# Performance work log

Hardware: AMD Instinct MI355X
Metric: run time of the kernel (lower is better)

Reference implementation:

```python
import jax, jax.numpy as jnp
import numpy as np

N0, N1, N2, K, D, H = 131072, 16384, 4096, 8, 256, 256
LN_EPS = 1e-5
BN_EPS = 1e-5


def _lstm_last(x, W_ih, W_hh, b_ih, b_hh):
    # x: [N, K, Din]; returns final hidden state [N, Hh] (DGL lstm aggregator)
    N = x.shape[0]
    Hh = W_hh.shape[1]

    def step(carry, xt):
        h, c = carry
        z = xt @ W_ih.T + b_ih + h @ W_hh.T + b_hh  # [N, 4*Hh]
        i, f, g, o = jnp.split(z, 4, axis=-1)
        c = jax.nn.sigmoid(f) * c + jax.nn.sigmoid(i) * jnp.tanh(g)
        h = jax.nn.sigmoid(o) * jnp.tanh(c)
        return (h, c), None

    init = (jnp.zeros((N, Hh), x.dtype), jnp.zeros((N, Hh), x.dtype))
    (h, _), _ = jax.lax.scan(step, init, jnp.swapaxes(x, 0, 1))
    return h


def _sage_lstm(h_src, idx, W_ih, W_hh, b_ih, b_hh, W_self, W_neigh, b_neigh):
    # DGL SAGEConv(aggregator='lstm'), eval mode (feat_drop = identity).
    n_dst = idx.shape[0]
    h_self = h_src[:n_dst]                  # DGL block: dst nodes are first rows of src
    nbrs = jnp.take(h_src, idx, axis=0)     # [n_dst, K, Din] neighbor gather
    h_n = _lstm_last(nbrs, W_ih, W_hh, b_ih, b_hh)
    # fc_self has no bias, fc_neigh has bias (DGL); activation = exact GELU
    return jax.nn.gelu(h_self @ W_self.T + h_n @ W_neigh.T + b_neigh, approximate=False)


def _layernorm(x, g, b):
    mu = jnp.mean(x, -1, keepdims=True)
    var = jnp.mean((x - mu) ** 2, -1, keepdims=True)
    return (x - mu) * jax.lax.rsqrt(var + LN_EPS) * g + b


def _forward(h0, idx0, idx1,
             W_ih1, W_hh1, b_ih1, b_hh1, W_self1, W_neigh1, b_neigh1,
             W_ih2, W_hh2, b_ih2, b_hh2, W_self2, W_neigh2, b_neigh2,
             ln_g, ln_b, bn_g, bn_b, bn_mean, bn_var, W1, b1, W2, b2):
    h = _sage_lstm(h0, idx0, W_ih1, W_hh1, b_ih1, b_hh1, W_self1, W_neigh1, b_neigh1)
    h = _layernorm(h, ln_g, ln_b)           # shared self.norm
    h = _sage_lstm(h, idx1, W_ih2, W_hh2, b_ih2, b_hh2, W_self2, W_neigh2, b_neigh2)
    h = _layernorm(h, ln_g, ln_b)
    # classifier head, eval mode: Dropout = identity, BatchNorm1d uses running stats
    h = (h - bn_mean) * jax.lax.rsqrt(bn_var + BN_EPS) * bn_g + bn_b
    h = jax.nn.gelu(h @ W1.T + b1, approximate=False)
    return h @ W2.T + b2                    # [N2, 1] logits


def setup_inputs() -> dict:
    key = jax.random.key(0)
    ks = jax.random.split(key, 24)

    def p(i, shape, scale=0.05):
        return jax.random.normal(ks[i], shape, jnp.float32) * scale

    return {
        "h0": jax.random.normal(ks[0], (N0, D), jnp.float32),
        "idx0": jax.random.randint(ks[1], (N1, K), 0, N0),
        "idx1": jax.random.randint(ks[2], (N2, K), 0, N1),
        "W_ih1": p(3, (4 * H, D)), "W_hh1": p(4, (4 * H, H)),
        "b_ih1": p(5, (4 * H,)), "b_hh1": p(6, (4 * H,)),
        "W_self1": p(7, (H, D)), "W_neigh1": p(8, (H, H)), "b_neigh1": p(9, (H,)),
        "W_ih2": p(10, (4 * H, H)), "W_hh2": p(11, (4 * H, H)),
        "b_ih2": p(12, (4 * H,)), "b_hh2": p(13, (4 * H,)),
        "W_self2": p(14, (H, H)), "W_neigh2": p(15, (H, H)), "b_neigh2": p(16, (H,)),
        "ln_g": jnp.ones((H,), jnp.float32), "ln_b": jnp.zeros((H,), jnp.float32),
        "bn_g": jnp.ones((H,), jnp.float32), "bn_b": jnp.zeros((H,), jnp.float32),
        "bn_mean": p(17, (H,)), "bn_var": jnp.ones((H,), jnp.float32),
        "W1": p(18, (H, H)), "b1": p(19, (H,)),
        "W2": p(20, (1, H)), "b2": p(21, (1,)),
    }


def reference(h0, idx0, idx1,
              W_ih1, W_hh1, b_ih1, b_hh1, W_self1, W_neigh1, b_neigh1,
              W_ih2, W_hh2, b_ih2, b_hh2, W_self2, W_neigh2, b_neigh2,
              ln_g, ln_b, bn_g, bn_b, bn_mean, bn_var, W1, b1, W2, b2):
    return _forward(h0, idx0, idx1,
                    W_ih1, W_hh1, b_ih1, b_hh1, W_self1, W_neigh1, b_neigh1,
                    W_ih2, W_hh2, b_ih2, b_hh2, W_self2, W_neigh2, b_neigh2,
                    ln_g, ln_b, bn_g, bn_b, bn_mean, bn_var, W1, b1, W2, b2)
```

## Files before the change

kernel.cpp:

```cpp
#include <hip/hip_runtime.h>
#include <hip/hip_bf16.h>
#include <math.h>

#define PN0 131072
#define PN1 16384
#define PN2 4096
#define PK  8

typedef __attribute__((ext_vector_type(8))) short short8;
typedef __attribute__((ext_vector_type(4))) float f32x4;

__device__ __forceinline__ unsigned pkbf2(float a, float b) {
  unsigned ua = __float_as_uint(a); ua = (ua + 0x7FFFu + ((ua >> 16) & 1u)) >> 16;
  unsigned ub = __float_as_uint(b); ub = (ub + 0x7FFFu + ((ub >> 16) & 1u)) >> 16;
  return ua | (ub << 16);
}
__device__ __forceinline__ unsigned short bf16r(float a) {
  unsigned ua = __float_as_uint(a);
  return (unsigned short)((ua + 0x7FFFu + ((ua >> 16) & 1u)) >> 16);
}
__device__ __forceinline__ float sigf(float x) { return 1.f / (1.f + __expf(-x)); }
__device__ __forceinline__ float tanh_fast(float x) { return 1.f - 2.f / (__expf(2.f * x) + 1.f); }
__device__ __forceinline__ float gelu_f(float v) {
  return 0.5f * v * (1.f + erff(v * 0.70710678118654752f));
}
__device__ __forceinline__ int permc(int n) {
  return (n & ~31) + (((n >> 2) & 3) * 8) + (((n >> 4) & 1) * 4) + (n & 3);
}

__device__ __forceinline__ void gload16(const void* g, void* l) {
  __builtin_amdgcn_global_load_lds(
      (const __attribute__((address_space(1))) void*)g,
      (__attribute__((address_space(3))) void*)l, 16, 0, 0);
}

__device__ __forceinline__ void dev_cvt_perm(int t, unsigned short* dst,
                                             const float* src) {
  int row = t >> 3, c0 = (t & 7) * 32;
  const float* s = src + (size_t)row * 256 + c0;
  unsigned short* d = dst + (size_t)row * 256 + c0;
  float f[32];
#pragma unroll
  for (int i = 0; i < 8; ++i) *(float4*)&f[i * 4] = *(const float4*)(s + i * 4);
#pragma unroll
  for (int q = 0; q < 4; ++q) {
    uint4 u;
    u.x = pkbf2(f[4 * q + 0], f[4 * q + 1]);
    u.y = pkbf2(f[4 * q + 2], f[4 * q + 3]);
    u.z = pkbf2(f[16 + 4 * q + 0], f[16 + 4 * q + 1]);
    u.w = pkbf2(f[16 + 4 * q + 2], f[16 + 4 * q + 3]);
    *(uint4*)(d + q * 8) = u;
  }
}

__device__ __forceinline__ void dev_pack_w(int t, unsigned short* dst,
                                           const float* Wih, const float* Whh) {
  int e = t & 7, slot = (t >> 3) & 3, row = (t >> 5) & 127;
  int kc = (t >> 12) & 15, tn = t >> 16;
  int q = slot ^ ((row >> 1) & 3);
  int k = kc * 32 + 16 * (e >> 2) + 4 * q + (e & 3);
  int hc = tn * 32 + ((row >> 6) << 4) + (row & 15);
  int g = (row >> 4) & 3;
  int n = g * 256 + hc;
  float v = (k < 256) ? Wih[(size_t)n * 256 + k] : Whh[(size_t)n * 256 + (k - 256)];
  dst[t] = bf16r(v);
}

__device__ __forceinline__ void dev_pack_plain(int t, unsigned short* dst,
                                               const float* A, const float* B, int nkc) {
  int e = t & 7, slot = (t >> 3) & 3, row = (t >> 5) & 127;
  int rest = t >> 12;
  int kc = rest % nkc, tn = rest / nkc;
  int q = slot ^ ((row >> 1) & 3);
  int k = kc * 32 + 16 * (e >> 2) + 4 * q + (e & 3);
  int n = tn * 128 + row;
  float v = (k < 256) ? A[(size_t)n * 256 + k] : B[(size_t)n * 256 + (k - 256)];
  dst[t] = bf16r(v);
}

__global__ __launch_bounds__(256) void prep_kernel(
    unsigned short* __restrict__ h0b, const float* __restrict__ h0,
    unsigned short* __restrict__ pB1, const float* __restrict__ Wih1, const float* __restrict__ Whh1,
    unsigned short* __restrict__ pB2, const float* __restrict__ Wih2, const float* __restrict__ Whh2,
    unsigned short* __restrict__ pC1, const float* __restrict__ Ws1, const float* __restrict__ Wn1,
    unsigned short* __restrict__ pC2, const float* __restrict__ Ws2, const float* __restrict__ Wn2,
    unsigned short* __restrict__ pM, const float* __restrict__ W1,
    float* __restrict__ bcat1, const float* __restrict__ bih1, const float* __restrict__ bhh1,
    float* __restrict__ bcat2, const float* __restrict__ bih2, const float* __restrict__ bhh2)
{
  const int b = blockIdx.x;
  const int tid = threadIdx.x;
  if (b < 4096) {
    dev_cvt_perm(b * 256 + tid, h0b, h0);
  } else if (b < 6144) {
    dev_pack_w((b - 4096) * 256 + tid, pB1, Wih1, Whh1);
  } else if (b < 8192) {
    dev_pack_w((b - 6144) * 256 + tid, pB2, Wih2, Whh2);
  } else if (b < 8704) {
    dev_pack_plain((b - 8192) * 256 + tid, pC1, Ws1, Wn1, 16);
  } else if (b < 9216) {
    dev_pack_plain((b - 8704) * 256 + tid, pC2, Ws2, Wn2, 16);
  } else if (b < 9472) {
    dev_pack_plain((b - 9216) * 256 + tid, pM, W1, W1, 8);
  } else {
    int i = (b - 9472) * 256 + tid;
    if (i < 1024) bcat1[i] = bih1[i] + bhh1[i];
    else          bcat2[i - 1024] = bih2[i - 1024] + bhh2[i - 1024];
  }
}

template<int MI>
__global__ __launch_bounds__(256) void lstm_step_t(
    const unsigned short* __restrict__ xb,
    const int* __restrict__ idx, int t,
    const unsigned short* __restrict__ hb_in,
    const unsigned short* __restrict__ packW,
    const float* __restrict__ bcat,
    float* __restrict__ cbuf,
    unsigned short* __restrict__ hb_out,
    int first)
{
  __shared__ short As[3][MI * 1024];
  __shared__ short Bs[3][4096];

  const int tid = threadIdx.x;
  const int l = tid & 63;
  const int w = tid >> 6;
  const int m0 = blockIdx.x * (MI * 32);
  const int tn = blockIdx.y;
  const int wm = w >> 1, wn = w & 1;

  const int q = (l & 3) ^ ((l >> 3) & 3);
  const int r0 = w * (MI * 8) + (l >> 2);
  const int m_a = m0 + r0;
  const unsigned short* xp0 = xb + (size_t)idx[(size_t)m_a * PK + t] * 256 + 8 * q;
  const unsigned short* hp0 = hb_in + (size_t)m_a * 256 + 8 * q;
  const unsigned short* xp1 = nullptr;
  const unsigned short* hp1 = nullptr;
  if constexpr (MI == 4) {
    const int m_b = m_a + 16;
    xp1 = xb + (size_t)idx[(size_t)m_b * PK + t] * 256 + 8 * q;
    hp1 = hb_in + (size_t)m_b * 256 + 8 * q;
  }
  const unsigned short* bp = packW + (size_t)tn * 65536 + (size_t)w * 1024 + (size_t)l * 8;

  f32x4 acc[MI][4];
#pragma unroll
  for (int mi = 0; mi < MI; ++mi)
#pragma unroll
    for (int ni = 0; ni < 4; ++ni) acc[mi][ni] = (f32x4)(0.f);

  auto STAGE = [&](int buf, int kc) {
    short* Ad = &As[buf][0];
    short* Bd = &Bs[buf][0];
    gload16(bp + (size_t)kc * 4096, Bd + w * 1024);
    gload16(bp + (size_t)kc * 4096 + 512, Bd + w * 1024 + 512);
    const unsigned short* s0 = (kc < 8) ? xp0 + kc * 32 : hp0 + (kc - 8) * 32;
    gload16(s0, Ad + w * (MI * 256));
    if constexpr (MI == 4) {
      const unsigned short* s1 = (kc < 8) ? xp1 + kc * 32 : hp1 + (kc - 8) * 32;
      gload16(s1, Ad + w * 1024 + 512);
    }
  };

  const int lr = l & 15;
  const int lq = l >> 4;
  const int slot_r = (lq ^ ((l >> 1) & 3)) * 8;

  auto COMPUTE = [&](int buf) {
    short8 af[MI], bf[4];
#pragma unroll
    for (int mi = 0; mi < MI; ++mi)
      af[mi] = *(const short8*)&As[buf][(wm * (MI * 16) + mi * 16 + lr) * 32 + slot_r];
#pragma unroll
    for (int ni = 0; ni < 4; ++ni)
      bf[ni] = *(const short8*)&Bs[buf][(wn * 64 + ni * 16 + lr) * 32 + slot_r];
#pragma unroll
    for (int mi = 0; mi < MI; ++mi)
#pragma unroll
      for (int ni = 0; ni < 4; ++ni)
        acc[mi][ni] = __builtin_amdgcn_mfma_f32_16x16x32_bf16(af[mi], bf[ni], acc[mi][ni], 0, 0, 0);
  };

  const int NK = first ? 8 : 16;
  STAGE(0, 0);
  STAGE(1, 1);
  for (int kc = 0; kc < NK; ++kc) {
    const int b0 = kc % 3;
    if (kc + 2 < NK) {
      STAGE((kc + 2) % 3, kc + 2);
      if constexpr (MI == 4) asm volatile("s_waitcnt vmcnt(8)" ::: "memory");
      else                   asm volatile("s_waitcnt vmcnt(6)" ::: "memory");
    } else if (kc + 1 < NK) {
      if constexpr (MI == 4) asm volatile("s_waitcnt vmcnt(4)" ::: "memory");
      else                   asm volatile("s_waitcnt vmcnt(3)" ::: "memory");
    } else {
      asm volatile("s_waitcnt vmcnt(0)" ::: "memory");
    }
    __builtin_amdgcn_s_barrier();
    asm volatile("" ::: "memory");
    COMPUTE(b0);
    asm volatile("" ::: "memory");
    if (kc + 1 < NK) __builtin_amdgcn_s_barrier();
  }

  const int hc = tn * 32 + wn * 16 + lr;
  const float bi = bcat[hc], bff = bcat[256 + hc], bg = bcat[512 + hc], bo = bcat[768 + hc];
  const int hpos = permc(hc);
#pragma unroll
  for (int mi = 0; mi < MI; ++mi) {
#pragma unroll
    for (int r = 0; r < 4; ++r) {
      const int m = m0 + wm * (MI * 16) + mi * 16 + lq * 4 + r;
      const size_t off = (size_t)m * 256;
      const float zi = acc[mi][0][r] + bi;
      const float zf = acc[mi][1][r] + bff;
      const float zg = acc[mi][2][r] + bg;
      const float zo = acc[mi][3][r] + bo;
      const float cp = first ? 0.f : cbuf[off + hc];
      const float cn = sigf(zf) * cp + sigf(zi) * tanh_fast(zg);
      const float hn = sigf(zo) * tanh_fast(cn);
      cbuf[off + hc] = cn;
      hb_out[off + hpos] = bf16r(hn);
    }
  }
}

__global__ __launch_bounds__(256) void combine_ln_kernel(
    const unsigned short* __restrict__ selfb,
    const unsigned short* __restrict__ neighb,
    const unsigned short* __restrict__ packW,
    const float* __restrict__ bias,
    unsigned short* __restrict__ outb,
    const float* __restrict__ g, const float* __restrict__ b,
    const float* bnm, const float* bnv, const float* bng, const float* bnb,
    int do_bn)
{
  __shared__ short As[2][1024];
  __shared__ short Bs[2][8192];

  const int tid = threadIdx.x;
  const int l = tid & 63;
  const int w = tid >> 6;
  const int m0 = blockIdx.x * 32;
  const int wm = w >> 1, wn = w & 1;

  const int q = (l & 3) ^ ((l >> 3) & 3);
  const int arow = (w & 1) * 16 + (l >> 2);
  const unsigned short* sp = selfb + (size_t)(m0 + arow) * 256 + 8 * q;
  const unsigned short* np = neighb + (size_t)(m0 + arow) * 256 + 8 * q;

  f32x4 acc[8];
#pragma unroll
  for (int ni = 0; ni < 8; ++ni) acc[ni] = (f32x4)(0.f);

  auto STAGE = [&](int buf, int kc) {
    short* Ad = &As[buf][0];
    short* Bd = &Bs[buf][0];
#pragma unroll
    for (int u = 0; u < 4; ++u) {
      const int base = w * 64 + u * 16;
      const int tile = base >> 7, r128b = base & 127;
      gload16(packW + (size_t)tile * 65536 + (size_t)kc * 4096 + (size_t)r128b * 32 + (size_t)l * 8,
              Bd + w * 2048 + u * 512);
    }
    if (w < 2) {
      const unsigned short* s0 = (kc < 8) ? sp + kc * 32 : np + (kc - 8) * 32;
      gload16(s0, Ad + w * 512);
    }
  };

  const int lr = l & 15;
  const int lq = l >> 4;
  const int slot_r = (lq ^ ((l >> 1) & 3)) * 8;

  auto COMPUTE = [&](int buf) {
    short8 af = *(const short8*)&As[buf][(wm * 16 + lr) * 32 + slot_r];
#pragma unroll
    for (int ni = 0; ni < 8; ++ni) {
      short8 bf = *(const short8*)&Bs[buf][(wn * 128 + ni * 16 + lr) * 32 + slot_r];
      acc[ni] = __builtin_amdgcn_mfma_f32_16x16x32_bf16(af, bf, acc[ni], 0, 0, 0);
    }
  };

  STAGE(0, 0);
  __syncthreads();
  for (int kc = 0; kc < 16; ++kc) {
    const int cur = kc & 1;
    if (kc + 1 < 16) STAGE(cur ^ 1, kc + 1);
    COMPUTE(cur);
    __syncthreads();
  }

  float val[8][4];
  float s[4] = {0.f, 0.f, 0.f, 0.f}, qq[4] = {0.f, 0.f, 0.f, 0.f};
#pragma unroll
  for (int ni = 0; ni < 8; ++ni) {
    const int n = wn * 128 + ni * 16 + lr;
    const float bb = bias[n];
#pragma unroll
    for (int r = 0; r < 4; ++r) {
      float v = gelu_f(acc[ni][r] + bb);
      val[ni][r] = v;
      s[r] += v;
      qq[r] += v * v;
    }
  }
#pragma unroll
  for (int off = 1; off < 16; off <<= 1) {
#pragma unroll
    for (int r = 0; r < 4; ++r) {
      s[r] += __shfl_xor(s[r], off);
      qq[r] += __shfl_xor(qq[r], off);
    }
  }
  float* sred = (float*)&As[0][0];
  __syncthreads();
  if (lr == 0) {
#pragma unroll
    for (int r = 0; r < 4; ++r) {
      const int row = wm * 16 + lq * 4 + r;
      sred[wn * 64 + row] = s[r];
      sred[wn * 64 + 32 + row] = qq[r];
    }
  }
  __syncthreads();
#pragma unroll
  for (int r = 0; r < 4; ++r) {
    const int row = wm * 16 + lq * 4 + r;
    const float S = sred[row] + sred[64 + row];
    const float Q = sred[32 + row] + sred[96 + row];
    const float mu = S * (1.f / 256.f);
    const float var = Q * (1.f / 256.f) - mu * mu;
    const float rs = rsqrtf(var + 1e-5f);
    const int m = m0 + row;
#pragma unroll
    for (int ni = 0; ni < 8; ++ni) {
      const int n = wn * 128 + ni * 16 + lr;
      float y = (val[ni][r] - mu) * rs * g[n] + b[n];
      if (do_bn) y = (y - bnm[n]) * rsqrtf(bnv[n] + 1e-5f) * bng[n] + bnb[n];
      outb[(size_t)m * 256 + permc(n)] = bf16r(y);
    }
  }
}

__global__ __launch_bounds__(256) void mlp_head_kernel(
    const unsigned short* __restrict__ h3b,
    const unsigned short* __restrict__ packM,
    const float* __restrict__ b1,
    const float* __restrict__ W2, const float* __restrict__ b2,
    float* __restrict__ out)
{
  __shared__ short As[2][1024];
  __shared__ short Bs[2][8192];

  const int tid = threadIdx.x;
  const int l = tid & 63;
  const int w = tid >> 6;
  const int m0 = blockIdx.x * 32;
  const int wm = w >> 1, wn = w & 1;

  const int q = (l & 3) ^ ((l >> 3) & 3);
  const int arow = (w & 1) * 16 + (l >> 2);
  const unsigned short* sp = h3b + (size_t)(m0 + arow) * 256 + 8 * q;

  f32x4 acc[8];
#pragma unroll
  for (int ni = 0; ni < 8; ++ni) acc[ni] = (f32x4)(0.f);

  auto STAGE = [&](int buf, int kc) {
    short* Ad = &As[buf][0];
    short* Bd = &Bs[buf][0];
#pragma unroll
    for (int u = 0; u < 4; ++u) {
      const int base = w * 64 + u * 16;
      const int tile = base >> 7, r128b = base & 127;
      gload16(packM + (size_t)tile * 32768 + (size_t)kc * 4096 + (size_t)r128b * 32 + (size_t)l * 8,
              Bd + w * 2048 + u * 512);
    }
    if (w < 2) gload16(sp + kc * 32, Ad + w * 512);
  };

  const int lr = l & 15;
  const int lq = l >> 4;
  const int slot_r = (lq ^ ((l >> 1) & 3)) * 8;

  auto COMPUTE = [&](int buf) {
    short8 af = *(const short8*)&As[buf][(wm * 16 + lr) * 32 + slot_r];
#pragma unroll
    for (int ni = 0; ni < 8; ++ni) {
      short8 bf = *(const short8*)&Bs[buf][(wn * 128 + ni * 16 + lr) * 32 + slot_r];
      acc[ni] = __builtin_amdgcn_mfma_f32_16x16x32_bf16(af, bf, acc[ni], 0, 0, 0);
    }
  };

  STAGE(0, 0);
  __syncthreads();
  for (int kc = 0; kc < 8; ++kc) {
    const int cur = kc & 1;
    if (kc + 1 < 8) STAGE(cur ^ 1, kc + 1);
    COMPUTE(cur);
    __syncthreads();
  }

  float s[4] = {0.f, 0.f, 0.f, 0.f};
#pragma unroll
  for (int ni = 0; ni < 8; ++ni) {
    const int n = wn * 128 + ni * 16 + lr;
    const float bb = b1[n];
    const float w2 = W2[n];
#pragma unroll
    for (int r = 0; r < 4; ++r) {
      s[r] += gelu_f(acc[ni][r] + bb) * w2;
    }
  }
#pragma unroll
  for (int off = 1; off < 16; off <<= 1)
#pragma unroll
    for (int r = 0; r < 4; ++r) s[r] += __shfl_xor(s[r], off);

  float* sred = (float*)&As[0][0];
  __syncthreads();
  if (lr == 0) {
#pragma unroll
    for (int r = 0; r < 4; ++r) sred[wn * 32 + wm * 16 + lq * 4 + r] = s[r];
  }
  __syncthreads();
  if (wn == 0 && lr == 0) {
#pragma unroll
    for (int r = 0; r < 4; ++r) {
      const int row = wm * 16 + lq * 4 + r;
      out[m0 + row] = sred[row] + sred[32 + row] + b2[0];
    }
  }
}

extern "C" void kernel_launch(void* const* d_in, const int* in_sizes, int n_in,
                              void* d_out, int out_size, void* d_ws, size_t ws_size,
                              hipStream_t stream) {
  const float* h0       = (const float*)d_in[0];
  const int*   idx0     = (const int*)  d_in[1];
  const int*   idx1     = (const int*)  d_in[2];
  const float* W_ih1    = (const float*)d_in[3];
  const float* W_hh1    = (const float*)d_in[4];
  const float* b_ih1    = (const float*)d_in[5];
  const float* b_hh1    = (const float*)d_in[6];
  const float* W_self1  = (const float*)d_in[7];
  const float* W_neigh1 = (const float*)d_in[8];
  const float* b_neigh1 = (const float*)d_in[9];
  const float* W_ih2    = (const float*)d_in[10];
  const float* W_hh2    = (const float*)d_in[11];
  const float* b_ih2    = (const float*)d_in[12];
  const float* b_hh2    = (const float*)d_in[13];
  const float* W_self2  = (const float*)d_in[14];
  const float* W_neigh2 = (const float*)d_in[15];
  const float* b_neigh2 = (const float*)d_in[16];
  const float* ln_g     = (const float*)d_in[17];
  const float* ln_b     = (const float*)d_in[18];
  const float* bn_g     = (const float*)d_in[19];
  const float* bn_b     = (const float*)d_in[20];
  const float* bn_mean  = (const float*)d_in[21];
  const float* bn_var   = (const float*)d_in[22];
  const float* W1       = (const float*)d_in[23];
  const float* b1       = (const float*)d_in[24];
  const float* W2       = (const float*)d_in[25];
  const float* b2       = (const float*)d_in[26];
  float* out = (float*)d_out;

  float* ws = (float*)d_ws;
  unsigned short* packB1 = (unsigned short*)ws;
  unsigned short* packB2 = (unsigned short*)(ws + 262144);
  unsigned short* packC1 = (unsigned short*)(ws + 524288);
  unsigned short* packC2 = (unsigned short*)(ws + 589824);
  unsigned short* packM  = (unsigned short*)(ws + 655360);
  float* bcat1 = ws + 688128;
  float* bcat2 = bcat1 + 1024;
  unsigned short* h0b = (unsigned short*)(bcat2 + 1024);
  float* afterh0 = (float*)h0b + 16777216;
  unsigned short* hbA = (unsigned short*)afterh0;
  unsigned short* hbB = (unsigned short*)(afterh0 + 2097152);
  float* cbuf = afterh0 + 4194304;
  unsigned short* h1b = (unsigned short*)(cbuf + 4194304);
  unsigned short* h3b = (unsigned short*)(cbuf + 4194304 + 2097152);

  prep_kernel<<<9480, 256, 0, stream>>>(
      h0b, h0,
      packB1, W_ih1, W_hh1,
      packB2, W_ih2, W_hh2,
      packC1, W_self1, W_neigh1,
      packC2, W_self2, W_neigh2,
      packM, W1,
      bcat1, b_ih1, b_hh1,
      bcat2, b_ih2, b_hh2);

  for (int t = 0; t < PK; ++t) {
    unsigned short* hin  = (t & 1) ? hbA : hbB;
    unsigned short* hout = (t & 1) ? hbB : hbA;
    lstm_step_t<4><<<dim3(PN1 / 128, 8), 256, 0, stream>>>(
        h0b, idx0, t, hin, packB1, bcat1, cbuf, hout, t == 0);
  }
  combine_ln_kernel<<<PN1 / 32, 256, 0, stream>>>(
      h0b, hbB, packC1, b_neigh1, h1b, ln_g, ln_b,
      nullptr, nullptr, nullptr, nullptr, 0);

  for (int t = 0; t < PK; ++t) {
    unsigned short* hin  = (t & 1) ? hbA : hbB;
    unsigned short* hout = (t & 1) ? hbB : hbA;
    lstm_step_t<2><<<dim3(PN2 / 64, 8), 256, 0, stream>>>(
        h1b, idx1, t, hin, packB2, bcat2, cbuf, hout, t == 0);
  }
  combine_ln_kernel<<<PN2 / 32, 256, 0, stream>>>(
      h1b, hbB, packC2, b_neigh2, h3b, ln_g, ln_b,
      bn_mean, bn_var, bn_g, bn_b, 1);
  mlp_head_kernel<<<PN2 / 32, 256, 0, stream>>>(h3b, packM, b1, W2, b2, out);
}
```

Before: 475.2 us.

## Fuse layer-2 LSTM steps into a persistent kernel with per-row-tile barriers

Replaces the eight per-timestep launches of the layer-2 LSTM with one persistent kernel. The 8 column blocks sharing a row tile synchronise through a global atomic counter, and the cell state stays in registers instead of going through cbuf. It also rewrites the layer-1 step kernel from a 3-stage pipeline with explicit vmcnt waits to a simpler double-buffered loop with __syncthreads. The persistent kernel relies on all 512 blocks being co-resident, or it can deadlock; the simpler layer-1 pipeline may lose some load/compute overlap.

```diff
diff --git a/kernel.cpp b/kernel.cpp
--- a/kernel.cpp
+++ b/kernel.cpp
@@ -86,7 +86,8 @@
     unsigned short* __restrict__ pC2, const float* __restrict__ Ws2, const float* __restrict__ Wn2,
     unsigned short* __restrict__ pM, const float* __restrict__ W1,
     float* __restrict__ bcat1, const float* __restrict__ bih1, const float* __restrict__ bhh1,
-    float* __restrict__ bcat2, const float* __restrict__ bih2, const float* __restrict__ bhh2)
+    float* __restrict__ bcat2, const float* __restrict__ bih2, const float* __restrict__ bhh2,
+    unsigned* __restrict__ bar)
 {
   const int b = blockIdx.x;
   const int tid = threadIdx.x;
@@ -102,15 +103,17 @@
     dev_pack_plain((b - 8704) * 256 + tid, pC2, Ws2, Wn2, 16);
   } else if (b < 9472) {
     dev_pack_plain((b - 9216) * 256 + tid, pM, W1, W1, 8);
-  } else {
+  } else if (b < 9480) {
     int i = (b - 9472) * 256 + tid;
     if (i < 1024) bcat1[i] = bih1[i] + bhh1[i];
     else          bcat2[i - 1024] = bih2[i - 1024] + bhh2[i - 1024];
-  }
-}
-
-template<int MI>
-__global__ __launch_bounds__(256) void lstm_step_t(
+  } else {
+#pragma unroll
+    for (int i = tid; i < 1024; i += 256) bar[i] = 0u;
+  }
+}
+
+__global__ __launch_bounds__(256) void lstm_step4_kernel(
     const unsigned short* __restrict__ xb,
     const int* __restrict__ idx, int t,
     const unsigned short* __restrict__ hb_in,
@@ -120,33 +123,29 @@
     unsigned short* __restrict__ hb_out,
     int first)
 {
-  __shared__ short As[3][MI * 1024];
-  __shared__ short Bs[3][4096];
+  __shared__ short As[2][4096];
+  __shared__ short Bs[2][4096];
 
   const int tid = threadIdx.x;
   const int l = tid & 63;
   const int w = tid >> 6;
-  const int m0 = blockIdx.x * (MI * 32);
+  const int m0 = blockIdx.x * 128;
   const int tn = blockIdx.y;
   const int wm = w >> 1, wn = w & 1;
 
   const int q = (l & 3) ^ ((l >> 3) & 3);
-  const int r0 = w * (MI * 8) + (l >> 2);
+  const int r0 = w * 32 + (l >> 2);
   const int m_a = m0 + r0;
+  const int m_b = m_a + 16;
   const unsigned short* xp0 = xb + (size_t)idx[(size_t)m_a * PK + t] * 256 + 8 * q;
+  const unsigned short* xp1 = xb + (size_t)idx[(size_t)m_b * PK + t] * 256 + 8 * q;
   const unsigned short* hp0 = hb_in + (size_t)m_a * 256 + 8 * q;
-  const unsigned short* xp1 = nullptr;
-  const unsigned short* hp1 = nullptr;
-  if constexpr (MI == 4) {
-    const int m_b = m_a + 16;
-    xp1 = xb + (size_t)idx[(size_t)m_b * PK + t] * 256 + 8 * q;
-    hp1 = hb_in + (size_t)m_b * 256 + 8 * q;
-  }
+  const unsigned short* hp1 = hb_in + (size_t)m_b * 256 + 8 * q;
   const unsigned short* bp = packW + (size_t)tn * 65536 + (size_t)w * 1024 + (size_t)l * 8;
 
-  f32x4 acc[MI][4];
-#pragma unroll
-  for (int mi = 0; mi < MI; ++mi)
+  f32x4 acc[4][4];
+#pragma unroll
+  for (int mi = 0; mi < 4; ++mi)
 #pragma unroll
     for (int ni = 0; ni < 4; ++ni) acc[mi][ni] = (f32x4)(0.f);
 
@@ -155,12 +154,11 @@
     short* Bd = &Bs[buf][0];
     gload16(bp + (size_t)kc * 4096, Bd + w * 1024);
     gload16(bp + (size_t)kc * 4096 + 512, Bd + w * 1024 + 512);
-    const unsigned short* s0 = (kc < 8) ? xp0 + kc * 32 : hp0 + (kc - 8) * 32;
-    gload16(s0, Ad + w * (MI * 256));
-    if constexpr (MI == 4) {
-      const unsigned short* s1 = (kc < 8) ? xp1 + kc * 32 : hp1 + (kc - 8) * 32;
-      gload16(s1, Ad + w * 1024 + 512);
-    }
+    const unsigned short *s0, *s1;
+    if (kc < 8) { s0 = xp0 + kc * 32; s1 = xp1 + kc * 32; }
+    else        { s0 = hp0 + (kc - 8) * 32; s1 = hp1 + (kc - 8) * 32; }
+    gload16(s0, Ad + w * 1024);
+    gload16(s1, Ad + w * 1024 + 512);
   };
 
   const int lr = l & 15;
@@ -168,15 +166,15 @@
   const int slot_r = (lq ^ ((l >> 1) & 3)) * 8;
 
   auto COMPUTE = [&](int buf) {
-    short8 af[MI], bf[4];
-#pragma unroll
-    for (int mi = 0; mi < MI; ++mi)
-      af[mi] = *(const short8*)&As[buf][(wm * (MI * 16) + mi * 16 + lr) * 32 + slot_r];
+    short8 af[4], bf[4];
+#pragma unroll
+    for (int mi = 0; mi < 4; ++mi)
+      af[mi] = *(const short8*)&As[buf][(wm * 64 + mi * 16 + lr) * 32 + slot_r];
 #pragma unroll
     for (int ni = 0; ni < 4; ++ni)
       bf[ni] = *(const short8*)&Bs[buf][(wn * 64 + ni * 16 + lr) * 32 + slot_r];
 #pragma unroll
-    for (int mi = 0; mi < MI; ++mi)
+    for (int mi = 0; mi < 4; ++mi)
 #pragma unroll
       for (int ni = 0; ni < 4; ++ni)
         acc[mi][ni] = __builtin_amdgcn_mfma_f32_16x16x32_bf16(af[mi], bf[ni], acc[mi][ni], 0, 0, 0);
@@ -184,34 +182,22 @@
 
   const int NK = first ? 8 : 16;
   STAGE(0, 0);
-  STAGE(1, 1);
+  __syncthreads();
   for (int kc = 0; kc < NK; ++kc) {
-    const int b0 = kc % 3;
-    if (kc + 2 < NK) {
-      STAGE((kc + 2) % 3, kc + 2);
-      if constexpr (MI == 4) asm volatile("s_waitcnt vmcnt(8)" ::: "memory");
-      else                   asm volatile("s_waitcnt vmcnt(6)" ::: "memory");
-    } else if (kc + 1 < NK) {
-      if constexpr (MI == 4) asm volatile("s_waitcnt vmcnt(4)" ::: "memory");
-      else                   asm volatile("s_waitcnt vmcnt(3)" ::: "memory");
-    } else {
-      asm volatile("s_waitcnt vmcnt(0)" ::: "memory");
-    }
-    __builtin_amdgcn_s_barrier();
-    asm volatile("" ::: "memory");
-    COMPUTE(b0);
-    asm volatile("" ::: "memory");
-    if (kc + 1 < NK) __builtin_amdgcn_s_barrier();
+    const int cur = kc & 1;
+    if (kc + 1 < NK) STAGE(cur ^ 1, kc + 1);
+    COMPUTE(cur);
+    __syncthreads();
   }
 
   const int hc = tn * 32 + wn * 16 + lr;
   const float bi = bcat[hc], bff = bcat[256 + hc], bg = bcat[512 + hc], bo = bcat[768 + hc];
   const int hpos = permc(hc);
 #pragma unroll
-  for (int mi = 0; mi < MI; ++mi) {
+  for (int mi = 0; mi < 4; ++mi) {
 #pragma unroll
     for (int r = 0; r < 4; ++r) {
-      const int m = m0 + wm * (MI * 16) + mi * 16 + lq * 4 + r;
+      const int m = m0 + wm * 64 + mi * 16 + lq * 4 + r;
       const size_t off = (size_t)m * 256;
       const float zi = acc[mi][0][r] + bi;
       const float zf = acc[mi][1][r] + bff;
@@ -222,6 +208,120 @@
       const float hn = sigf(zo) * tanh_fast(cn);
       cbuf[off + hc] = cn;
       hb_out[off + hpos] = bf16r(hn);
+    }
+  }
+}
+
+__global__ __launch_bounds__(256) void lstm2_persist_kernel(
+    const unsigned short* __restrict__ xb,
+    const int* __restrict__ idx,
+    const unsigned short* __restrict__ packW,
+    const float* __restrict__ bcat,
+    unsigned short* __restrict__ hbA,
+    unsigned short* __restrict__ hbB,
+    unsigned* __restrict__ bar)
+{
+  __shared__ short As[2][2048];
+  __shared__ short Bs[2][4096];
+
+  const int tid = threadIdx.x;
+  const int l = tid & 63;
+  const int w = tid >> 6;
+  const int m0 = blockIdx.x * 64;
+  const int tn = blockIdx.y;
+  const int wm = w >> 1, wn = w & 1;
+
+  const int q = (l & 3) ^ ((l >> 3) & 3);
+  const int r0 = w * 16 + (l >> 2);
+  const int m_a = m0 + r0;
+  const unsigned short* bp = packW + (size_t)tn * 65536 + (size_t)w * 1024 + (size_t)l * 8;
+
+  const int lr = l & 15;
+  const int lq = l >> 4;
+  const int slot_r = (lq ^ ((l >> 1) & 3)) * 8;
+
+  const int hc = tn * 32 + wn * 16 + lr;
+  const float bi = bcat[hc], bff = bcat[256 + hc], bg = bcat[512 + hc], bo = bcat[768 + hc];
+  const int hpos = permc(hc);
+
+  unsigned* myctr = bar + blockIdx.x * 16;
+
+  float cst[8];
+#pragma unroll
+  for (int i = 0; i < 8; ++i) cst[i] = 0.f;
+
+  for (int t = 0; t < PK; ++t) {
+    const unsigned short* hin = (t & 1) ? hbA : hbB;
+    unsigned short* hout = (t & 1) ? hbB : hbA;
+    const unsigned short* xp0 = xb + (size_t)idx[(size_t)m_a * PK + t] * 256 + 8 * q;
+    const unsigned short* hp0 = hin + (size_t)m_a * 256 + 8 * q;
+
+    f32x4 acc[2][4];
+#pragma unroll
+    for (int mi = 0; mi < 2; ++mi)
+#pragma unroll
+      for (int ni = 0; ni < 4; ++ni) acc[mi][ni] = (f32x4)(0.f);
+
+    auto STAGE = [&](int buf, int kc) {
+      short* Ad = &As[buf][0];
+      short* Bd = &Bs[buf][0];
+      gload16(bp + (size_t)kc * 4096, Bd + w * 1024);
+      gload16(bp + (size_t)kc * 4096 + 512, Bd + w * 1024 + 512);
+      const unsigned short* s0 = (kc < 8) ? xp0 + kc * 32 : hp0 + (kc - 8) * 32;
+      gload16(s0, Ad + w * 512);
+    };
+
+    auto COMPUTE = [&](int buf) {
+      short8 af[2], bf[4];
+#pragma unroll
+      for (int mi = 0; mi < 2; ++mi)
+        af[mi] = *(const short8*)&As[buf][(wm * 32 + mi * 16 + lr) * 32 + slot_r];
+#pragma unroll
+      for (int ni = 0; ni < 4; ++ni)
+        bf[ni] = *(const short8*)&Bs[buf][(wn * 64 + ni * 16 + lr) * 32 + slot_r];
+#pragma unroll
+      for (int mi = 0; mi < 2; ++mi)
+#pragma unroll
+        for (int ni = 0; ni < 4; ++ni)
+          acc[mi][ni] = __builtin_amdgcn_mfma_f32_16x16x32_bf16(af[mi], bf[ni], acc[mi][ni], 0, 0, 0);
+    };
+
+    const int NK = (t == 0) ? 8 : 16;
+    STAGE(0, 0);
+    __syncthreads();
+    for (int kc = 0; kc < NK; ++kc) {
+      const int cur = kc & 1;
+      if (kc + 1 < NK) STAGE(cur ^ 1, kc + 1);
+      COMPUTE(cur);
+      __syncthreads();
+    }
+
+#pragma unroll
+    for (int mi = 0; mi < 2; ++mi) {
+#pragma unroll
+      for (int r = 0; r < 4; ++r) {
+        const int m = m0 + wm * 32 + mi * 16 + lq * 4 + r;
+        const float zi = acc[mi][0][r] + bi;
+        const float zf = acc[mi][1][r] + bff;
+        const float zg = acc[mi][2][r] + bg;
+        const float zo = acc[mi][3][r] + bo;
+        const float cn = sigf(zf) * cst[mi * 4 + r] + sigf(zi) * tanh_fast(zg);
+        cst[mi * 4 + r] = cn;
+        hout[(size_t)m * 256 + hpos] = bf16r(sigf(zo) * tanh_fast(cn));
+      }
+    }
+
+    if (t < PK - 1) {
+      __threadfence();
+      __syncthreads();
+      if (tid == 0) {
+        __hip_atomic_fetch_add(myctr, 1u, __ATOMIC_RELEASE, __HIP_MEMORY_SCOPE_AGENT);
+        const unsigned tgt = 8u * (unsigned)(t + 1);
+        while (__hip_atomic_load(myctr, __ATOMIC_ACQUIRE, __HIP_MEMORY_SCOPE_AGENT) < tgt)
+          __builtin_amdgcn_s_sleep(1);
+      }
+      __syncthreads();
+      __threadfence();
     }
   }
 }
@@ -475,7 +575,8 @@
   unsigned short* packM  = (unsigned short*)(ws + 655360);
   float* bcat1 = ws + 688128;
   float* bcat2 = bcat1 + 1024;
-  unsigned short* h0b = (unsigned short*)(bcat2 + 1024);
+  unsigned* bar = (unsigned*)(bcat2 + 1024);
+  unsigned short* h0b = (unsigned short*)(bcat2 + 2048);
   float* afterh0 = (float*)h0b + 16777216;
   unsigned short* hbA = (unsigned short*)afterh0;
   unsigned short* hbB = (unsigned short*)(afterh0 + 2097152);
@@ -483,7 +584,7 @@
   unsigned short* h1b = (unsigned short*)(cbuf + 4194304);
   unsigned short* h3b = (unsigned short*)(cbuf + 4194304 + 2097152);
 
-  prep_kernel<<<9480, 256, 0, stream>>>(
+  prep_kernel<<<9481, 256, 0, stream>>>(
       h0b, h0,
       packB1, W_ih1, W_hh1,
       packB2, W_ih2, W_hh2,
@@ -491,24 +592,22 @@
       packC2, W_self2, W_neigh2,
       packM, W1,
       bcat1, b_ih1, b_hh1,
-      bcat2, b_ih2, b_hh2);
+      bcat2, b_ih2, b_hh2,
+      bar);
 
   for (int t = 0; t < PK; ++t) {
     unsigned short* hin  = (t & 1) ? hbA : hbB;
     unsigned short* hout = (t & 1) ? hbB : hbA;
-    lstm_step_t<4><<<dim3(PN1 / 128, 8), 256, 0, stream>>>(
+    lstm_step4_kernel<<<dim3(PN1 / 128, 8), 256, 0, stream>>>(
         h0b, idx0, t, hin, packB1, bcat1, cbuf, hout, t == 0);
   }
   combine_ln_kernel<<<PN1 / 32, 256, 0, stream>>>(
       h0b, hbB, packC1, b_neigh1, h1b, ln_g, ln_b,
       nullptr, nullptr, nullptr, nullptr, 0);
 
-  for (int t = 0; t < PK; ++t) {
-    unsigned short* hin  = (t & 1) ? hbA : hbB;
-    unsigned short* hout = (t & 1) ? hbB : hbA;
-    lstm_step_t<2><<<dim3(PN2 / 64, 8), 256, 0, stream>>>(
-        h1b, idx1, t, hin, packB2, bcat2, cbuf, hout, t == 0);
-  }
+  lstm2_persist_kernel<<<dim3(PN2 / 64, 8), 256, 0, stream>>>(
+      h1b, idx1, packB2, bcat2, hbA, hbB, bar);
+
   combine_ln_kernel<<<PN2 / 32, 256, 0, stream>>>(
       h1b, hbB, packC2, b_neigh2, h3b, ln_g, ln_b,
       bn_mean, bn_var, bn_g, bn_b, 1);
```

Measured after the change: 1.051 ms. +121.2%, slower.

## Load LSTM GEMM operands directly from global into registers, dropping LDS staging

Applied to the files above, without the earlier changes.

The LSTM step kernel no longer stages A (gathered neighbor features and hidden state) and B (packed weights) through a triple-buffered LDS pipeline with barriers. Each lane now reads its MFMA fragments straight from global memory, and the weight packing drops its LDS bank-swizzle to match. The K loop is split into fully unrolled x and h phases, and the h phase is skipped on the first step. This removes barriers and LDS traffic, but each wave now fetches redundant copies of shared tiles and relies on cache hits and compiler scheduling to hide global latency.

```diff
diff --git a/kernel.cpp b/kernel.cpp
--- a/kernel.cpp
+++ b/kernel.cpp
@@ -55,9 +55,8 @@
 
 __device__ __forceinline__ void dev_pack_w(int t, unsigned short* dst,
                                            const float* Wih, const float* Whh) {
-  int e = t & 7, slot = (t >> 3) & 3, row = (t >> 5) & 127;
+  int e = t & 7, q = (t >> 3) & 3, row = (t >> 5) & 127;
   int kc = (t >> 12) & 15, tn = t >> 16;
-  int q = slot ^ ((row >> 1) & 3);
   int k = kc * 32 + 16 * (e >> 2) + 4 * q + (e & 3);
   int hc = tn * 32 + ((row >> 6) << 4) + (row & 15);
   int g = (row >> 4) & 3;
@@ -120,88 +119,67 @@
     unsigned short* __restrict__ hb_out,
     int first)
 {
-  __shared__ short As[3][MI * 1024];
-  __shared__ short Bs[3][4096];
-
   const int tid = threadIdx.x;
   const int l = tid & 63;
   const int w = tid >> 6;
   const int m0 = blockIdx.x * (MI * 32);
   const int tn = blockIdx.y;
   const int wm = w >> 1, wn = w & 1;
-
-  const int q = (l & 3) ^ ((l >> 3) & 3);
-  const int r0 = w * (MI * 8) + (l >> 2);
-  const int m_a = m0 + r0;
-  const unsigned short* xp0 = xb + (size_t)idx[(size_t)m_a * PK + t] * 256 + 8 * q;
-  const unsigned short* hp0 = hb_in + (size_t)m_a * 256 + 8 * q;
-  const unsigned short* xp1 = nullptr;
-  const unsigned short* hp1 = nullptr;
-  if constexpr (MI == 4) {
-    const int m_b = m_a + 16;
-    xp1 = xb + (size_t)idx[(size_t)m_b * PK + t] * 256 + 8 * q;
-    hp1 = hb_in + (size_t)m_b * 256 + 8 * q;
-  }
-  const unsigned short* bp = packW + (size_t)tn * 65536 + (size_t)w * 1024 + (size_t)l * 8;
-
-  f32x4 acc[MI][4];
-#pragma unroll
-  for (int mi = 0; mi < MI; ++mi)
-#pragma unroll
-    for (int ni = 0; ni < 4; ++ni) acc[mi][ni] = (f32x4)(0.f);
-
-  auto STAGE = [&](int buf, int kc) {
-    short* Ad = &As[buf][0];
-    short* Bd = &Bs[buf][0];
-    gload16(bp + (size_t)kc * 4096, Bd + w * 1024);
-    gload16(bp + (size_t)kc * 4096 + 512, Bd + w * 1024 + 512);
-    const unsigned short* s0 = (kc < 8) ? xp0 + kc * 32 : hp0 + (kc - 8) * 32;
-    gload16(s0, Ad + w * (MI * 256));
-    if constexpr (MI == 4) {
-      const unsigned short* s1 = (kc < 8) ? xp1 + kc * 32 : hp1 + (kc - 8) * 32;
-      gload16(s1, Ad + w * 1024 + 512);
-    }
-  };
-
   const int lr = l & 15;
   const int lq = l >> 4;
-  const int slot_r = (lq ^ ((l >> 1) & 3)) * 8;
-
-  auto COMPUTE = [&](int buf) {
+
+  const unsigned short* xr[MI];
+  const unsigned short* hr[MI];
+#pragma unroll
+  for (int mi = 0; mi < MI; ++mi) {
+    const int m = m0 + wm * (MI * 16) + mi * 16 + lr;
+    xr[mi] = xb + (size_t)idx[(size_t)m * PK + t] * 256 + lq * 8;
+    hr[mi] = hb_in + (size_t)m * 256 + lq * 8;
+  }
+  const unsigned short* br[4];
+#pragma unroll
+  for (int ni = 0; ni < 4; ++ni) {
+    const int nrow = wn * 64 + ni * 16 + lr;
+    br[ni] = packW + (size_t)tn * 65536 + (size_t)nrow * 32 + lq * 8;
+  }
+
+  f32x4 acc[MI][4];
+#pragma unroll
+  for (int mi = 0; mi < MI; ++mi)
+#pragma unroll
+    for (int ni = 0; ni < 4; ++ni) acc[mi][ni] = (f32x4)(0.f);
+
+#pragma unroll
+  for (int kc = 0; kc < 8; ++kc) {
     short8 af[MI], bf[4];
 #pragma unroll
     for (int mi = 0; mi < MI; ++mi)
-      af[mi] = *(const short8*)&As[buf][(wm * (MI * 16) + mi * 16 + lr) * 32 + slot_r];
+      af[mi] = *(const short8*)(xr[mi] + kc * 32);
 #pragma unroll
     for (int ni = 0; ni < 4; ++ni)
-      bf[ni] = *(const short8*)&Bs[buf][(wn * 64 + ni * 16 + lr) * 32 + slot_r];
+      bf[ni] = *(const short8*)(br[ni] + (size_t)kc * 4096);
 #pragma unroll
     for (int mi = 0; mi < MI; ++mi)
 #pragma unroll
       for (int ni = 0; ni < 4; ++ni)
         acc[mi][ni] = __builtin_amdgcn_mfma_f32_16x16x32_bf16(af[mi], bf[ni], acc[mi][ni], 0, 0, 0);
-  };
-
-  const int NK = first ? 8 : 16;
-  STAGE(0, 0);
-  STAGE(1, 1);
-  for (int kc = 0; kc < NK; ++kc) {
-    const int b0 = kc % 3;
-    if (kc + 2 < NK) {
-      STAGE((kc + 2) % 3, kc + 2);
-      if constexpr (MI == 4) asm volatile("s_waitcnt vmcnt(8)" ::: "memory");
-      else                   asm volatile("s_waitcnt vmcnt(6)" ::: "memory");
-    } else if (kc + 1 < NK) {
-      if constexpr (MI == 4) asm volatile("s_waitcnt vmcnt(4)" ::: "memory");
-      else                   asm volatile("s_waitcnt vmcnt(3)" ::: "memory");
-    } else {
-      asm volatile("s_waitcnt vmcnt(0)" ::: "memory");
-    }
-    __builtin_amdgcn_s_barrier();
-    asm volatile("" ::: "memory");
-    COMPUTE(b0);
-    asm volatile("" ::: "memory");
-    if (kc + 1 < NK) __builtin_amdgcn_s_barrier();
+  }
+  if (!first) {
+#pragma unroll
+    for (int kc = 0; kc < 8; ++kc) {
+      short8 af[MI], bf[4];
+#pragma unroll
+      for (int mi = 0; mi < MI; ++mi)
+        af[mi] = *(const short8*)(hr[mi] + kc * 32);
+#pragma unroll
+      for (int ni = 0; ni < 4; ++ni)
+        bf[ni] = *(const short8*)(br[ni] + (size_t)(kc + 8) * 4096);
+#pragma unroll
+      for (int mi = 0; mi < MI; ++mi)
+#pragma unroll
+        for (int ni = 0; ni < 4; ++ni)
+          acc[mi][ni] = __builtin_amdgcn_mfma_f32_16x16x32_bf16(af[mi], bf[ni], acc[mi][ni], 0, 0, 0);
+    }
   }
 
   const int hc = tn * 32 + wn * 16 + lr;
```

Result: slower. 693.0 us (+45.8%).
